# Kernel tuning notes

Measured on AMD Instinct MI355X. Metric: run time of the kernel, lower is better.

## Reference

```python
import jax, jax.numpy as jnp
import numpy as np

D = 50  # hidden size hardcoded in the module

def setup_inputs() -> dict:
    key = jax.random.key(0)
    ks = jax.random.split(key, 12)
    B, T = 4096, 1024
    s = 0.1
    return {
        "input": jax.random.normal(ks[0], (B, T, 2), dtype=jnp.float32),
        # LSTMCell 1: input size 2 -> hidden 50, gate order i,f,g,o (4*D rows)
        "W_ih1": jax.random.normal(ks[1], (4 * D, 2), dtype=jnp.float32) * s,
        "W_hh1": jax.random.normal(ks[2], (4 * D, D), dtype=jnp.float32) * s,
        "b_ih1": jax.random.normal(ks[3], (4 * D,), dtype=jnp.float32) * s,
        "b_hh1": jax.random.normal(ks[4], (4 * D,), dtype=jnp.float32) * s,
        # LSTMCell 2: hidden 50 -> hidden 50
        "W_ih2": jax.random.normal(ks[5], (4 * D, D), dtype=jnp.float32) * s,
        "W_hh2": jax.random.normal(ks[6], (4 * D, D), dtype=jnp.float32) * s,
        "b_ih2": jax.random.normal(ks[7], (4 * D,), dtype=jnp.float32) * s,
        "b_hh2": jax.random.normal(ks[8], (4 * D,), dtype=jnp.float32) * s,
        # Linear: 50 -> 2
        "W_lin": jax.random.normal(ks[9], (2, D), dtype=jnp.float32) * s,
        "b_lin": jax.random.normal(ks[10], (2,), dtype=jnp.float32) * s,
    }

def _lstm_cell(x, h, c, W_ih, W_hh, b_ih, b_hh):
    # gates: [B, 4D], torch LSTMCell gate order i, f, g, o
    gates = x @ W_ih.T + b_ih + h @ W_hh.T + b_hh
    i, f, g, o = jnp.split(gates, 4, axis=-1)
    c_new = jax.nn.sigmoid(f) * c + jax.nn.sigmoid(i) * jnp.tanh(g)
    h_new = jax.nn.sigmoid(o) * jnp.tanh(c_new)
    return h_new, c_new

def reference(input, W_ih1, W_hh1, b_ih1, b_hh1, W_ih2, W_hh2, b_ih2, b_hh2, W_lin, b_lin):
    B = input.shape[0]
    dt = input.dtype
    zeros = jnp.zeros((B, D), dtype=dt)

    def step(carry, x_t):
        h1, c1, h2, c2 = carry
        h1, c1 = _lstm_cell(x_t, h1, c1, W_ih1, W_hh1, b_ih1, b_hh1)
        h2, c2 = _lstm_cell(h1, h2, c2, W_ih2, W_hh2, b_ih2, b_hh2)
        out = h2 @ W_lin.T + b_lin  # [B, 2]
        return (h1, c1, h2, c2), out

    xs = jnp.swapaxes(input, 0, 1)  # [T, B, 2]
    _, outs = jax.lax.scan(step, (zeros, zeros, zeros, zeros), xs)
    return jnp.swapaxes(outs, 0, 1)  # [B, T, 2] (squeeze(2) is a no-op since size is 2)
```

## Files before the change

### kernel.cpp

```cpp
#include <hip/hip_runtime.h>
#include <stdint.h>

#define DD 50
#define TT 1024
#define NB 16
#define KF 32

typedef _Float16 half_t;
typedef __attribute__((ext_vector_type(8))) _Float16 f16x8;
typedef __attribute__((ext_vector_type(4))) float    f32x4;

#define AHS 72
#define A2S 72
#define OBW 68

__device__ __forceinline__ float rcp_f(float x)  { return __builtin_amdgcn_rcpf(x); }
__device__ __forceinline__ float exp2_f(float x) { return __builtin_amdgcn_exp2f(x); }

__device__ __forceinline__ float cell_update(const f32x4 acc, float& c) {
    const float a   = exp2_f(-1.4426950f * acc[0]);
    const float b   = exp2_f( 2.8853901f * acc[2]);
    const float t   = 1.0f + a;
    const float pig = (b - 1.0f) * rcp_f(t + t * b);
    const float pf  = rcp_f(1.0f + exp2_f(-1.4426950f * acc[1]));
    const float cn  = pf * c + pig;
    c = cn;
    const float o_  = exp2_f(-1.4426950f * acc[3]);
    const float e   = exp2_f( 2.8853901f * cn);
    const float t2  = 1.0f + o_;
    return (e - 1.0f) * rcp_f(t2 + t2 * e);
}


__global__ __launch_bounds__(512, 2)
void lstm_mfma_kernel(const float* __restrict__ x,
                      const float* __restrict__ W_ih1, const float* __restrict__ W_hh1,
                      const float* __restrict__ b_ih1, const float* __restrict__ b_hh1,
                      const float* __restrict__ W_ih2, const float* __restrict__ W_hh2,
                      const float* __restrict__ b_ih2, const float* __restrict__ b_hh2,
                      const float* __restrict__ W_lin, const float* __restrict__ b_lin,
                      float* __restrict__ out)
{
    const int tid  = threadIdx.x;
    const int lane = tid & 63;
    const int w    = tid >> 6;
    const int bg0  = blockIdx.x * NB;
    const int cl   = lane & 15;
    const int g2   = lane >> 4;

    __shared__ half_t AH[2][NB][AHS];
    __shared__ half_t A2[2][NB][A2S];
    __shared__ float  obuf[2][NB][OBW];
    __shared__ float  xbuf[2][NB][KF*2];

    const int cnt   = (w < 5) ? 2 : 1;
    const int tbase = (w < 5) ? 2 * w : 5 + w;

    f16x8 b1f[2][2];
    f16x8 b2f[2][4];
#pragma unroll
    for (int i = 0; i < 2; ++i) {
        const int  colp  = (tbase + i) * 16 + cl;
        const bool valid = (colp < 200) && (i < cnt);
        const bool headB = ((colp == 200) || (colp == 201)) && (i < cnt);
        const int  g     = (colp & 3) * DD + (colp >> 2);
#pragma unroll
        for (int kt = 0; kt < 2; ++kt)
#pragma unroll
            for (int j = 0; j < 8; ++j) {
                const int k = kt * 32 + g2 * 8 + j;
                float v = 0.f;
                if (valid) {
                    if (k < DD)          v = W_hh1[g * DD + k];
                    else if (k < DD + 2) v = W_ih1[g * 2 + (k - DD)];
                    else if (k == 52)    v = b_ih1[g] + b_hh1[g];
                }
                b1f[i][kt][j] = (half_t)v;
            }
#pragma unroll
        for (int kt = 0; kt < 2; ++kt)
#pragma unroll
            for (int j = 0; j < 8; ++j) {
                const int k = kt * 32 + g2 * 8 + j;
                float v = 0.f;
                if (k < DD) {
                    if (valid) v = W_ih2[g * DD + k];
                } else if (k == 52) {
                    if (valid)      v = b_ih2[g] + b_hh2[g];
                    else if (headB) v = b_lin[colp - 200];
                }
                b2f[i][kt][j] = (half_t)v;
            }
#pragma unroll
        for (int kt = 2; kt < 4; ++kt)
#pragma unroll
            for (int j = 0; j < 8; ++j) {
                const int kk = (kt - 2) * 32 + g2 * 8 + j;
                float v = 0.f;
                if (kk < DD) {
                    if (valid)      v = W_hh2[g * DD + kk];
                    else if (headB) v = W_lin[(colp - 200) * DD + kk];
                }
                b2f[i][kt][j] = (half_t)v;
            }
    }

    for (int idx = tid; idx < 2 * NB * AHS; idx += 512) ((half_t*)AH)[idx] = (half_t)0.f;
    for (int idx = tid; idx < 2 * NB * A2S; idx += 512) ((half_t*)A2)[idx] = (half_t)0.f;
    if (tid >= 256) {
        const int idx = tid - 256, xr = idx >> 4, xq = idx & 15;
        const f32x4 v = *(const f32x4*)(x + (size_t)(bg0 + xr) * (TT * 2) + xq * 4);
        *(f32x4*)&xbuf[0][xr][xq * 4] = v;
    }
    __syncthreads();
    if (tid < NB) {
        AH[0][tid][52] = (half_t)1.0f; AH[1][tid][52] = (half_t)1.0f;
        AH[1][tid][50] = (half_t)xbuf[0][tid][0];
        AH[1][tid][51] = (half_t)xbuf[0][tid][1];
    }
    __syncthreads();

    float c1r[2] = {0.f, 0.f};
    float c2r[2] = {0.f, 0.f};

    for (int I = -1; I <= TT; ++I) {
        const int p  = I & 1;
        const int np = p ^ 1;

        if (((I & 31) == 1) && I >= 33 && tid >= 256) {
            const int fr = (tid - 256) >> 4, fq = (tid - 256) & 15;
            const f32x4 v = *(const f32x4*)&obuf[((I - 33) >> 5) & 1][fr][fq * 4];
            *(f32x4*)(out + (size_t)(bg0 + fr) * (TT * 2) + (I - 33) * 2 + fq * 4) = v;
        }
        f32x4 xpre; bool hp = false;
        if (I >= 0 && ((I & 31) == 0) && tid >= 256) {
            const int chunk = (I >> 5) + 1;
            if (chunk < TT / KF) {
                hp = true;
                const int idx = tid - 256, xr = idx >> 4, xq = idx & 15;
                xpre = *(const f32x4*)(x + (size_t)(bg0 + xr) * (TT * 2) + chunk * (KF * 2) + xq * 4);
            }
        }

        const f16x8 a0 = *(const f16x8*)&AH[p][cl][g2 * 8];
        const f16x8 a1 = *(const f16x8*)&AH[p][cl][32 + g2 * 8];
        const f16x8 h0 = *(const f16x8*)&A2[p][cl][g2 * 8];
        const f16x8 h1 = *(const f16x8*)&A2[p][cl][32 + g2 * 8];

        f32x4 acc2[2];
        if (I >= 0) {
#pragma unroll
            for (int i = 0; i < 2; ++i) {
                f32x4 z = {0.f,0.f,0.f,0.f};
                if (i < cnt) {
                    z = __builtin_amdgcn_mfma_f32_16x16x32_f16(b2f[i][2], h0, z, 0, 0, 0);
                    z = __builtin_amdgcn_mfma_f32_16x16x32_f16(b2f[i][3], h1, z, 0, 0, 0);
                    z = __builtin_amdgcn_mfma_f32_16x16x32_f16(b2f[i][0], a0, z, 0, 0, 0);
                    z = __builtin_amdgcn_mfma_f32_16x16x32_f16(b2f[i][1], a1, z, 0, 0, 0);
                }
                acc2[i] = z;
            }
        }
        f32x4 acc1[2];
        if (I < TT) {
#pragma unroll
            for (int i = 0; i < 2; ++i) {
                f32x4 z = {0.f,0.f,0.f,0.f};
                if (i < cnt) {
                    z = __builtin_amdgcn_mfma_f32_16x16x32_f16(b1f[i][0], a0, z, 0, 0, 0);
                    z = __builtin_amdgcn_mfma_f32_16x16x32_f16(b1f[i][1], a1, z, 0, 0, 0);
                }
                acc1[i] = z;
            }
        }

        if (I >= 0) {
            if (I < TT) {
#pragma unroll
                for (int i = 0; i < 2; ++i) {
                    const int jj = (tbase + i) * 4 + g2;
                    if (i < cnt && jj < DD)
                        A2[np][cl][jj] = (half_t)cell_update(acc2[i], c2r[i]);
                }
            }
            if (w == 7 && g2 == 2 && I >= 1) {
                const int s = I - 1;
                obuf[(s >> 5) & 1][cl][(s & 31) * 2 + 0] = acc2[0][0];
                obuf[(s >> 5) & 1][cl][(s & 31) * 2 + 1] = acc2[0][1];
            }
        }
        if (I < TT) {
#pragma unroll
            for (int i = 0; i < 2; ++i) {
                const int jj = (tbase + i) * 4 + g2;
                if (i < cnt && jj < DD)
                    AH[np][cl][jj] = (half_t)cell_update(acc1[i], c1r[i]);
            }
            if (w == 7 && g2 == 3 && (I + 2) < TT) {
                const int r = lane - 48, tn = I + 2;
                const float* xs = &xbuf[(tn >> 5) & 1][r][(tn & 31) * 2];
                AH[np][r][50] = (half_t)xs[0];
                AH[np][r][51] = (half_t)xs[1];
            }
            if (hp) {
                const int idx = tid - 256, xr = idx >> 4, xq = idx & 15;
                *(f32x4*)&xbuf[(((I >> 5) + 1) & 1)][xr][xq * 4] = xpre;
            }
        }
        __syncthreads();
    }

    if (tid >= 256) {
        const int fr = (tid - 256) >> 4, fq = (tid - 256) & 15;
        const f32x4 v = *(const f32x4*)&obuf[1][fr][fq * 4];
        *(f32x4*)(out + (size_t)(bg0 + fr) * (TT * 2) + (TT - KF) * 2 + fq * 4) = v;
    }
}

extern "C" void kernel_launch(void* const* d_in, const int* in_sizes, int n_in,
                              void* d_out, int out_size, void* d_ws, size_t ws_size,
                              hipStream_t stream) {
    const float* x     = (const float*)d_in[0];
    const float* W_ih1 = (const float*)d_in[1];
    const float* W_hh1 = (const float*)d_in[2];
    const float* b_ih1 = (const float*)d_in[3];
    const float* b_hh1 = (const float*)d_in[4];
    const float* W_ih2 = (const float*)d_in[5];
    const float* W_hh2 = (const float*)d_in[6];
    const float* b_ih2 = (const float*)d_in[7];
    const float* b_hh2 = (const float*)d_in[8];
    const float* W_lin = (const float*)d_in[9];
    const float* b_lin = (const float*)d_in[10];
    float* out = (float*)d_out;

    const int B = in_sizes[0] / (TT * 2);
    const int blocks = B / NB;

    hipLaunchKernelGGL(lstm_mfma_kernel, dim3(blocks), dim3(512), 0, stream,
                       x, W_ih1, W_hh1, b_ih1, b_hh1,
                       W_ih2, W_hh2, b_ih2, b_hh2, W_lin, b_lin, out);
}
```

Baseline: 890.0 us.

## Spread gate tiles across 16 waves with one tile per wave

Doubles the block to 1024 threads so each of 13 compute waves owns a single 16-column gate tile instead of up to two. This shortens the per-step critical path of MFMAs and cell updates. Loads and stores of x and out move to waves 12-15. The time loop is unrolled by two so the double-buffer parity is a compile-time constant. The cost is one resident block per CU instead of two, and a barrier over 16 waves every step, which may lower overall throughput.

```diff
diff --git a/kernel.cpp b/kernel.cpp
--- a/kernel.cpp
+++ b/kernel.cpp
@@ -32,7 +32,7 @@
 }
 
 
-__global__ __launch_bounds__(512, 2)
+__global__ __launch_bounds__(1024, 1)
 void lstm_mfma_kernel(const float* __restrict__ x,
                       const float* __restrict__ W_ih1, const float* __restrict__ W_hh1,
                       const float* __restrict__ b_ih1, const float* __restrict__ b_hh1,
@@ -53,16 +53,19 @@
     __shared__ float  obuf[2][NB][OBW];
     __shared__ float  xbuf[2][NB][KF*2];
 
-    const int cnt   = (w < 5) ? 2 : 1;
-    const int tbase = (w < 5) ? 2 * w : 5 + w;
-
-    f16x8 b1f[2][2];
-    f16x8 b2f[2][4];
-#pragma unroll
-    for (int i = 0; i < 2; ++i) {
-        const int  colp  = (tbase + i) * 16 + cl;
-        const bool valid = (colp < 200) && (i < cnt);
-        const bool headB = ((colp == 200) || (colp == 201)) && (i < cnt);
+    const bool isComp = (w < 13);
+    const int  tile   = isComp ? w : 0;
+    const int  jj     = tile * 4 + g2;
+    const bool doUpd  = isComp && (jj < DD);
+    const bool headLn = (w == 12) && (g2 == 2);
+    const int  xr     = (tid - 768) >> 4;
+    const int  xq     = tid & 15;
+
+    f16x8 b1f[2], b2f[4];
+    {
+        const int  colp  = tile * 16 + cl;
+        const bool valid = isComp && (colp < 200);
+        const bool headB = isComp && (colp >= 200) && (colp <= 201);
         const int  g     = (colp & 3) * DD + (colp >> 2);
 #pragma unroll
         for (int kt = 0; kt < 2; ++kt)
@@ -75,7 +78,7 @@
                     else if (k < DD + 2) v = W_ih1[g * 2 + (k - DD)];
                     else if (k == 52)    v = b_ih1[g] + b_hh1[g];
                 }
-                b1f[i][kt][j] = (half_t)v;
+                b1f[kt][j] = (half_t)v;
             }
 #pragma unroll
         for (int kt = 0; kt < 2; ++kt)
@@ -89,7 +92,7 @@
                     if (valid)      v = b_ih2[g] + b_hh2[g];
                     else if (headB) v = b_lin[colp - 200];
                 }
-                b2f[i][kt][j] = (half_t)v;
+                b2f[kt][j] = (half_t)v;
             }
 #pragma unroll
         for (int kt = 2; kt < 4; ++kt)
@@ -101,14 +104,13 @@
                     if (valid)      v = W_hh2[g * DD + kk];
                     else if (headB) v = W_lin[(colp - 200) * DD + kk];
                 }
-                b2f[i][kt][j] = (half_t)v;
+                b2f[kt][j] = (half_t)v;
             }
     }
 
-    for (int idx = tid; idx < 2 * NB * AHS; idx += 512) ((half_t*)AH)[idx] = (half_t)0.f;
-    for (int idx = tid; idx < 2 * NB * A2S; idx += 512) ((half_t*)A2)[idx] = (half_t)0.f;
-    if (tid >= 256) {
-        const int idx = tid - 256, xr = idx >> 4, xq = idx & 15;
+    for (int idx = tid; idx < 2 * NB * AHS; idx += 1024) ((half_t*)AH)[idx] = (half_t)0.f;
+    for (int idx = tid; idx < 2 * NB * A2S; idx += 1024) ((half_t*)A2)[idx] = (half_t)0.f;
+    if (tid >= 768) {
         const f32x4 v = *(const f32x4*)(x + (size_t)(bg0 + xr) * (TT * 2) + xq * 4);
         *(f32x4*)&xbuf[0][xr][xq * 4] = v;
     }
@@ -120,100 +122,74 @@
     }
     __syncthreads();
 
-    float c1r[2] = {0.f, 0.f};
-    float c2r[2] = {0.f, 0.f};
-
-    for (int I = -1; I <= TT; ++I) {
-        const int p  = I & 1;
-        const int np = p ^ 1;
-
-        if (((I & 31) == 1) && I >= 33 && tid >= 256) {
-            const int fr = (tid - 256) >> 4, fq = (tid - 256) & 15;
-            const f32x4 v = *(const f32x4*)&obuf[((I - 33) >> 5) & 1][fr][fq * 4];
-            *(f32x4*)(out + (size_t)(bg0 + fr) * (TT * 2) + (I - 33) * 2 + fq * 4) = v;
-        }
-        f32x4 xpre; bool hp = false;
-        if (I >= 0 && ((I & 31) == 0) && tid >= 256) {
-            const int chunk = (I >> 5) + 1;
-            if (chunk < TT / KF) {
-                hp = true;
-                const int idx = tid - 256, xr = idx >> 4, xq = idx & 15;
-                xpre = *(const f32x4*)(x + (size_t)(bg0 + xr) * (TT * 2) + chunk * (KF * 2) + xq * 4);
-            }
-        }
-
-        const f16x8 a0 = *(const f16x8*)&AH[p][cl][g2 * 8];
-        const f16x8 a1 = *(const f16x8*)&AH[p][cl][32 + g2 * 8];
-        const f16x8 h0 = *(const f16x8*)&A2[p][cl][g2 * 8];
-        const f16x8 h1 = *(const f16x8*)&A2[p][cl][32 + g2 * 8];
-
-        f32x4 acc2[2];
-        if (I >= 0) {
-#pragma unroll
-            for (int i = 0; i < 2; ++i) {
-                f32x4 z = {0.f,0.f,0.f,0.f};
-                if (i < cnt) {
-                    z = __builtin_amdgcn_mfma_f32_16x16x32_f16(b2f[i][2], h0, z, 0, 0, 0);
-                    z = __builtin_amdgcn_mfma_f32_16x16x32_f16(b2f[i][3], h1, z, 0, 0, 0);
-                    z = __builtin_amdgcn_mfma_f32_16x16x32_f16(b2f[i][0], a0, z, 0, 0, 0);
-                    z = __builtin_amdgcn_mfma_f32_16x16x32_f16(b2f[i][1], a1, z, 0, 0, 0);
-                }
-                acc2[i] = z;
-            }
-        }
-        f32x4 acc1[2];
-        if (I < TT) {
-#pragma unroll
-            for (int i = 0; i < 2; ++i) {
-                f32x4 z = {0.f,0.f,0.f,0.f};
-                if (i < cnt) {
-                    z = __builtin_amdgcn_mfma_f32_16x16x32_f16(b1f[i][0], a0, z, 0, 0, 0);
-                    z = __builtin_amdgcn_mfma_f32_16x16x32_f16(b1f[i][1], a1, z, 0, 0, 0);
-                }
-                acc1[i] = z;
-            }
-        }
-
-        if (I >= 0) {
-            if (I < TT) {
-#pragma unroll
-                for (int i = 0; i < 2; ++i) {
-                    const int jj = (tbase + i) * 4 + g2;
-                    if (i < cnt && jj < DD)
-                        A2[np][cl][jj] = (half_t)cell_update(acc2[i], c2r[i]);
-                }
-            }
-            if (w == 7 && g2 == 2 && I >= 1) {
-                const int s = I - 1;
-                obuf[(s >> 5) & 1][cl][(s & 31) * 2 + 0] = acc2[0][0];
-                obuf[(s >> 5) & 1][cl][(s & 31) * 2 + 1] = acc2[0][1];
-            }
-        }
-        if (I < TT) {
-#pragma unroll
-            for (int i = 0; i < 2; ++i) {
-                const int jj = (tbase + i) * 4 + g2;
-                if (i < cnt && jj < DD)
-                    AH[np][cl][jj] = (half_t)cell_update(acc1[i], c1r[i]);
-            }
-            if (w == 7 && g2 == 3 && (I + 2) < TT) {
-                const int r = lane - 48, tn = I + 2;
-                const float* xs = &xbuf[(tn >> 5) & 1][r][(tn & 31) * 2];
-                AH[np][r][50] = (half_t)xs[0];
-                AH[np][r][51] = (half_t)xs[1];
-            }
-            if (hp) {
-                const int idx = tid - 256, xr = idx >> 4, xq = idx & 15;
-                *(f32x4*)&xbuf[(((I >> 5) + 1) & 1)][xr][xq * 4] = xpre;
-            }
-        }
-        __syncthreads();
-    }
-
-    if (tid >= 256) {
-        const int fr = (tid - 256) >> 4, fq = (tid - 256) & 15;
-        const f32x4 v = *(const f32x4*)&obuf[1][fr][fq * 4];
-        *(f32x4*)(out + (size_t)(bg0 + fr) * (TT * 2) + (TT - KF) * 2 + fq * 4) = v;
+    float c1 = 0.f, c2 = 0.f;
+
+#define LSTM_STEP(PC)                                                              \
+    {                                                                               \
+        constexpr int P = (PC), NP = (PC) ^ 1;                                      \
+        if (((I & 31) == 1) && I >= 33 && tid >= 768) {                             \
+            const f32x4 v = *(const f32x4*)&obuf[((I - 33) >> 5) & 1][xr][xq * 4];  \
+            *(f32x4*)(out + (size_t)(bg0 + xr) * (TT * 2) + (I - 33) * 2 + xq * 4) = v; \
+        }                                                                           \
+        f32x4 xpre; bool hp = false;                                                \
+        if (((I & 31) == 0) && I >= 0 && tid >= 768) {                              \
+            const int chunk = (I >> 5) + 1;                                         \
+            if (chunk < TT / KF) {                                                  \
+                hp = true;                                                          \
+                xpre = *(const f32x4*)(x + (size_t)(bg0 + xr) * (TT * 2) + chunk * (KF * 2) + xq * 4); \
+            }                                                                       \
+        }                                                                           \
+        f32x4 acc1, acc2;                                                           \
+        if (isComp) {                                                               \
+            const f16x8 a0 = *(const f16x8*)&AH[P][cl][g2 * 8];                     \
+            const f16x8 a1 = *(const f16x8*)&AH[P][cl][32 + g2 * 8];                \
+            const f16x8 h0 = *(const f16x8*)&A2[P][cl][g2 * 8];                     \
+            const f16x8 h1 = *(const f16x8*)&A2[P][cl][32 + g2 * 8];                \
+            if (I >= 0) {                                                           \
+                f32x4 z = {0.f, 0.f, 0.f, 0.f};                                     \
+                z = __builtin_amdgcn_mfma_f32_16x16x32_f16(b2f[2], h0, z, 0, 0, 0); \
+                z = __builtin_amdgcn_mfma_f32_16x16x32_f16(b2f[3], h1, z, 0, 0, 0); \
+                z = __builtin_amdgcn_mfma_f32_16x16x32_f16(b2f[0], a0, z, 0, 0, 0); \
+                z = __builtin_amdgcn_mfma_f32_16x16x32_f16(b2f[1], a1, z, 0, 0, 0); \
+                acc2 = z;                                                           \
+            }                                                                       \
+            if (I < TT) {                                                           \
+                f32x4 z = {0.f, 0.f, 0.f, 0.f};                                     \
+                z = __builtin_amdgcn_mfma_f32_16x16x32_f16(b1f[0], a0, z, 0, 0, 0); \
+                z = __builtin_amdgcn_mfma_f32_16x16x32_f16(b1f[1], a1, z, 0, 0, 0); \
+                acc1 = z;                                                           \
+            }                                                                       \
+        }                                                                           \
+        if (I >= 0) {                                                               \
+            if (I < TT && doUpd) A2[NP][cl][jj] = (half_t)cell_update(acc2, c2);    \
+            if (headLn && I >= 1) {                                                 \
+                const int s = I - 1;                                                \
+                obuf[(s >> 5) & 1][cl][(s & 31) * 2 + 0] = acc2[0];                 \
+                obuf[(s >> 5) & 1][cl][(s & 31) * 2 + 1] = acc2[1];                 \
+            }                                                                       \
+        }                                                                           \
+        if (I < TT) {                                                               \
+            if (doUpd) AH[NP][cl][jj] = (half_t)cell_update(acc1, c1);              \
+            if (w == 13 && lane < 16 && (I + 2) < TT) {                             \
+                const int tn = I + 2;                                               \
+                const float* xs = &xbuf[(tn >> 5) & 1][lane][(tn & 31) * 2];        \
+                AH[NP][lane][50] = (half_t)xs[0];                                   \
+                AH[NP][lane][51] = (half_t)xs[1];                                   \
+            }                                                                       \
+            if (hp) *(f32x4*)&xbuf[((I >> 5) + 1) & 1][xr][xq * 4] = xpre;          \
+        }                                                                           \
+        __syncthreads();                                                            \
+    }
+
+    for (int I = -1; I <= TT; ) {
+        LSTM_STEP(1); ++I;
+        LSTM_STEP(0); ++I;
+    }
+#undef LSTM_STEP
+
+    if (tid >= 768) {
+        const f32x4 v = *(const f32x4*)&obuf[1][xr][xq * 4];
+        *(f32x4*)(out + (size_t)(bg0 + xr) * (TT * 2) + (TT - KF) * 2 + xq * 4) = v;
     }
 }
 
@@ -236,7 +212,7 @@
     const int B = in_sizes[0] / (TT * 2);
     const int blocks = B / NB;
 
-    hipLaunchKernelGGL(lstm_mfma_kernel, dim3(blocks), dim3(512), 0, stream,
+    hipLaunchKernelGGL(lstm_mfma_kernel, dim3(blocks), dim3(1024), 0, stream,
                        x, W_ih1, W_hh1, b_ih1, b_hh1,
                        W_ih2, W_hh2, b_ih2, b_hh2, W_lin, b_lin, out);
 }
```

After: 796.1 us (median of 2 runs). 10.6% less time.
